# Performance work log

Measured on AMD Instinct MI355X. Metric: run time of the kernel, lower is better.

## Reference

```python
import jax, jax.numpy as jnp
import numpy as np

NUM_USERS = 60000
NUM_ITEMS = 40000
N_NODES = NUM_USERS + NUM_ITEMS
EMBED_K = 128
E_HALF = 1_000_000  # bipartite interactions; symmetrized -> 2M directed edges


def setup_inputs() -> dict:
    key = jax.random.key(0)
    k1, k2, k3, k4, k5, k6, k7 = jax.random.split(key, 7)
    scale = 1.0 / np.sqrt(EMBED_K)  # ~ xavier_normal
    Gu = jax.random.normal(k1, (NUM_USERS, EMBED_K), jnp.float32) * scale
    Gi = jax.random.normal(k2, (NUM_ITEMS, EMBED_K), jnp.float32) * scale
    W0 = jax.random.normal(k3, (EMBED_K, EMBED_K), jnp.float32) * scale
    W1 = jax.random.normal(k4, (EMBED_K, EMBED_K), jnp.float32) * scale
    W2 = jax.random.normal(k5, (EMBED_K, EMBED_K), jnp.float32) * scale
    # bipartite user-item graph, symmetrized (items offset by NUM_USERS)
    u = jax.random.randint(k6, (E_HALF,), 0, NUM_USERS)
    it = jax.random.randint(k7, (E_HALF,), 0, NUM_ITEMS) + NUM_USERS
    src = jnp.concatenate([u, it])
    dst = jnp.concatenate([it, u])
    edge_index = jnp.stack([src, dst]).astype(jnp.int32)  # [2, 2M]
    return {"Gu": Gu, "Gi": Gi, "W0": W0, "W1": W1, "W2": W2,
            "edge_index": edge_index}


def reference(Gu, Gi, W0, W1, W2, edge_index):
    # add_self_loops=False, bias=False) -> ReLU), then split into (gu, gi).
    src, dst = edge_index[0], edge_index[1]
    n_users = Gu.shape[0]
    n_nodes = Gu.shape[0] + Gi.shape[0]
    # PyG gcn_norm (no self loops): deg = scatter(1, col); norm = d^-1/2[row]*d^-1/2[col]
    ones = jnp.ones(src.shape, Gu.dtype)
    deg = jax.ops.segment_sum(ones, dst, num_segments=n_nodes)
    dinv = jnp.where(deg > 0, jax.lax.rsqrt(jnp.maximum(deg, 1.0)), 0.0)
    norm = dinv[src] * dinv[dst]  # [E]
    x = jnp.concatenate([Gu, Gi], axis=0)  # [N, d]
    for W in (W0, W1, W2):
        h = x @ W                                   # [N, d] dense GEMM
        msg = h[src] * norm[:, None]                # [E, d] gather + scale
        x = jax.nn.relu(jax.ops.segment_sum(msg, dst, num_segments=n_nodes))
    return x[:n_users], x[n_users:]
```

## Files before the change

kernel.cpp:

```cpp
#include <hip/hip_runtime.h>
#include <hip/hip_bf16.h>

#define EMB 128
#define NPB 256
#define NB_PAD 512
#define CHUNK 4096
#define FILL_CAP 7168

typedef unsigned int uint32;
typedef unsigned long long uint64;
typedef __attribute__((ext_vector_type(8))) short bf16x8;
typedef __attribute__((ext_vector_type(4))) float f32x4;
typedef __attribute__((ext_vector_type(2))) float f32x2;
typedef __attribute__((ext_vector_type(2))) unsigned int uint32x2;

__device__ __forceinline__ ushort f2bf(float f) {
    uint32 u = __float_as_uint(f);
    return (ushort)((u + 0x7fff + ((u >> 16) & 1)) >> 16);
}
__device__ __forceinline__ uint32 pack_hi2(uint32 u0, uint32 u1) {
    return (u1 & 0xffff0000u) | (u0 >> 16);
}
__device__ __forceinline__ float blo(uint32 u) { return __uint_as_float(u << 16); }
__device__ __forceinline__ float bhi(uint32 u) { return __uint_as_float(u & 0xffff0000u); }


__global__ __launch_bounds__(256) void bucket_count_kernel(
    const int* __restrict__ dst, int* __restrict__ bucket_cnt, int E, int NB) {
    __shared__ int cnt[NB_PAD];
    int t = threadIdx.x;
    long e0 = (long)blockIdx.x * CHUNK;
    int n = E - (int)e0; if (n > CHUNK) n = CHUNK;
    for (int b = t; b < NB_PAD; b += 256) cnt[b] = 0;
    __syncthreads();
    #pragma unroll
    for (int i = 0; i < CHUNK / 256; i++) {
        int idx = t + i * 256;
        if (idx < n) atomicAdd(&cnt[dst[e0 + idx] >> 8], 1);
    }
    __syncthreads();
    for (int b = t; b < NB; b += 256)
        if (cnt[b] > 0) atomicAdd(&bucket_cnt[b], cnt[b]);
}

__global__ void bucket_scan_kernel(const int* __restrict__ bucket_cnt,
                                   int* __restrict__ ebase, int* __restrict__ gcursor,
                                   int NB, int E) {
    __shared__ int sc[512];
    int t = threadIdx.x;
    int v = (t < NB) ? bucket_cnt[t] : 0;
    sc[t] = v;
    __syncthreads();
    for (int off = 1; off < 512; off <<= 1) {
        int u = (t >= off) ? sc[t - off] : 0;
        __syncthreads();
        sc[t] += u;
        __syncthreads();
    }
    if (t < NB) {
        int excl = sc[t] - v;
        ebase[t] = excl;
        gcursor[t] = excl;
    }
    if (t == 0) ebase[NB] = E;
}


__global__ __launch_bounds__(256) void bucket_scatter_kernel(
    const int* __restrict__ src, const int* __restrict__ dst,
    int* __restrict__ gcursor, uint2* __restrict__ ebuf, int E, int NB) {
    __shared__ int cnt[NB_PAD];
    __shared__ int loff[NB_PAD];
    __shared__ int gbase[NB_PAD];
    __shared__ int pos[NB_PAD];
    __shared__ int sc[256];
    __shared__ uint2 stage[CHUNK];
    int t = threadIdx.x;
    long e0 = (long)blockIdx.x * CHUNK;
    int n = E - (int)e0; if (n > CHUNK) n = CHUNK;
    for (int b = t; b < NB_PAD; b += 256) { cnt[b] = 0; pos[b] = 0; }
    __syncthreads();
    int es[CHUNK / 256], ed[CHUNK / 256];
    #pragma unroll
    for (int i = 0; i < CHUNK / 256; i++) {
        int idx = t + i * 256;
        if (idx < n) {
            es[i] = src[e0 + idx];
            ed[i] = dst[e0 + idx];
            atomicAdd(&cnt[ed[i] >> 8], 1);
        }
    }
    __syncthreads();
    int a = cnt[2 * t], b2 = cnt[2 * t + 1];
    sc[t] = a + b2;
    __syncthreads();
    for (int off = 1; off < 256; off <<= 1) {
        int v = (t >= off) ? sc[t - off] : 0;
        __syncthreads();
        sc[t] += v;
        __syncthreads();
    }
    int excl = sc[t] - (a + b2);
    loff[2 * t] = excl;
    loff[2 * t + 1] = excl + a;
    __syncthreads();
    for (int b = t; b < NB; b += 256)
        if (cnt[b] > 0) gbase[b] = atomicAdd(&gcursor[b], cnt[b]);
    __syncthreads();
    #pragma unroll
    for (int i = 0; i < CHUNK / 256; i++) {
        int idx = t + i * 256;
        if (idx < n) {
            int b = ed[i] >> 8;
            int p = atomicAdd(&pos[b], 1);
            stage[loff[b] + p] = make_uint2((uint32)es[i], (uint32)ed[i]);
        }
    }
    __syncthreads();
    for (int i = t; i < n; i += 256) {
        uint2 e = stage[i];
        int b = (int)e.y >> 8;
        ebuf[gbase[b] + (i - loff[b])] = e;
    }
}


__global__ __launch_bounds__(256) void bucket_deg_kernel(
    const uint2* __restrict__ ebuf, const int* __restrict__ ebase,
    int* __restrict__ deg, float* __restrict__ dinv, int N) {
    __shared__ int cnt[NPB];
    int t = threadIdx.x;
    int n0 = blockIdx.x * NPB;
    int nn = N - n0; if (nn > NPB) nn = NPB;
    cnt[t] = 0;
    __syncthreads();
    int e0 = ebase[blockIdx.x];
    int e1 = ebase[blockIdx.x + 1];
    for (int e = e0 + t; e < e1; e += 256) {
        uint2 sd = ebuf[e];
        atomicAdd(&cnt[(int)sd.y - n0], 1);
    }
    __syncthreads();
    if (t < nn) {
        int c = cnt[t];
        deg[n0 + t] = c;
        dinv[n0 + t] = c > 0 ? rsqrtf((float)c) : 0.0f;
    }
}


__global__ void scan1_kernel(const int* __restrict__ deg, int* __restrict__ rowptr,
                             int* __restrict__ bsum, int N) {
    __shared__ int sc[256];
    int t = threadIdx.x;
    int base = blockIdx.x * 1024 + t * 4;
    int d0 = 0, d1 = 0, d2 = 0, d3 = 0;
    if (base + 3 < N) {
        int4 v = *(const int4*)(deg + base);
        d0 = v.x; d1 = v.y; d2 = v.z; d3 = v.w;
    } else {
        if (base     < N) d0 = deg[base];
        if (base + 1 < N) d1 = deg[base + 1];
        if (base + 2 < N) d2 = deg[base + 2];
        if (base + 3 < N) d3 = deg[base + 3];
    }
    int s = d0 + d1 + d2 + d3;
    sc[t] = s;
    __syncthreads();
    for (int off = 1; off < 256; off <<= 1) {
        int v = (t >= off) ? sc[t - off] : 0;
        __syncthreads();
        sc[t] += v;
        __syncthreads();
    }
    int excl = sc[t] - s;
    if (t == 255) bsum[blockIdx.x] = sc[255];
    int dd[4] = {d0, d1, d2, d3};
    int p = excl;
    #pragma unroll
    for (int j = 0; j < 4; j++) {
        int i = base + j;
        if (i < N) rowptr[i] = p;
        p += dd[j];
    }
}

__global__ void scan2_kernel(int* bsum, int nb) {
    __shared__ int sc[128];
    int t = threadIdx.x;
    int v = (t < nb) ? bsum[t] : 0;
    sc[t] = v;
    __syncthreads();
    for (int off = 1; off < 128; off <<= 1) {
        int u = (t >= off) ? sc[t - off] : 0;
        __syncthreads();
        sc[t] += u;
        __syncthreads();
    }
    if (t < nb) bsum[t] = sc[t] - v;
}

__global__ void scan3_kernel(int* __restrict__ rowptr, const int* __restrict__ bsum,
                             int N, int E) {
    int t = threadIdx.x, b = blockIdx.x;
    int add = bsum[b];
    int base = b * 1024 + t * 4;
    #pragma unroll
    for (int j = 0; j < 4; j++) {
        int i = base + j;
        if (i < N) rowptr[i] += add;
    }
    if (b == 0 && t == 0) rowptr[N] = E;
}


__global__ __launch_bounds__(256) void fill_ew_kernel(
    uint2* __restrict__ ebuf, const int* __restrict__ rowptr,
    const float* __restrict__ dinv, int N) {
    __shared__ uint2 stage[FILL_CAP];
    __shared__ int cnt[NPB];
    __shared__ int rp[NPB];
    int t = threadIdx.x;
    int n0 = blockIdx.x * NPB;
    int nn = N - n0; if (nn > NPB) nn = NPB;
    if (t < nn) { cnt[t] = 0; rp[t] = rowptr[n0 + t]; }
    __syncthreads();
    int e0 = rowptr[n0];
    int e1 = rowptr[n0 + nn];
    int ecount = e1 - e0; if (ecount > FILL_CAP) ecount = FILL_CAP;
    for (int o = t; o < ecount; o += 256) stage[o] = ebuf[e0 + o];
    __syncthreads();
    for (int o = t; o < ecount; o += 1024) {
        uint2 sd[4]; int pos[4]; float wv[4];
        int valid = 0;
        #pragma unroll
        for (int k = 0; k < 4; k++) {
            int oo = o + k * 256;
            if (oo < ecount) { sd[k] = stage[oo]; valid = k + 1; }
        }
        #pragma unroll
        for (int k = 0; k < 4; k++)
            if (k < valid) {
                int local = (int)sd[k].y - n0;
                pos[k] = rp[local] + atomicAdd(&cnt[local], 1);
            }
        #pragma unroll
        for (int k = 0; k < 4; k++)
            if (k < valid) wv[k] = dinv[(int)sd[k].x];
        #pragma unroll
        for (int k = 0; k < 4; k++)
            if (k < valid) ebuf[pos[k]] = make_uint2(sd[k].x, __float_as_uint(wv[k]));
    }
}


template<int DI>
__device__ __forceinline__ void agg_tail2(
    const uint32x2* __restrict__ Yh2, const uint2* __restrict__ ew,
    int base, int e0, int e1, int half, int l32,
    float& a0, float& a1, float& a2, float& a3) {
    uint32 rows[DI]; float w[DI]; uint32x2 p[DI];
    #pragma unroll
    for (int k = 0; k < DI; k++) {
        int i0 = base + 2 * k, i1 = i0 + 1;
        uint2 s0 = ew[i0 < e1 ? i0 : e0];
        uint2 s1 = ew[i1 < e1 ? i1 : e0];
        rows[k] = half ? s1.x : s0.x;
        uint32 wu = half ? s1.y : s0.y;
        w[k] = (i0 + half < e1) ? __uint_as_float(wu) : 0.0f;
    }
    #pragma unroll
    for (int k = 0; k < DI; k++) p[k] = Yh2[(size_t)rows[k] * 32 + l32];
    #pragma unroll
    for (int k = 0; k < DI; k++) {
        a0 += w[k] * blo(p[k].x); a1 += w[k] * bhi(p[k].x);
        a2 += w[k] * blo(p[k].y); a3 += w[k] * bhi(p[k].y);
    }
}

__device__ __forceinline__ void agg_node2(
    const uint32x2* __restrict__ Yh2, const uint2* __restrict__ ew,
    int e0, int e1, int half, int l32,
    float& a0, float& a1, float& a2, float& a3) {
    int base = e0;
    for (; base + 16 <= e1; base += 16) {
        uint32 rows[8]; float w[8]; uint32x2 p[8];
        #pragma unroll
        for (int k = 0; k < 8; k++) {
            uint2 s0 = ew[base + 2 * k];
            uint2 s1 = ew[base + 2 * k + 1];
            rows[k] = half ? s1.x : s0.x;
            w[k] = __uint_as_float(half ? s1.y : s0.y);
        }
        #pragma unroll
        for (int k = 0; k < 8; k++) p[k] = Yh2[(size_t)rows[k] * 32 + l32];
        #pragma unroll
        for (int k = 0; k < 8; k++) {
            a0 += w[k] * blo(p[k].x); a1 += w[k] * bhi(p[k].x);
            a2 += w[k] * blo(p[k].y); a3 += w[k] * bhi(p[k].y);
        }
    }
    int rem = e1 - base;
    if (rem > 8)      agg_tail2<8>(Yh2, ew, base, e0, e1, half, l32, a0, a1, a2, a3);
    else if (rem > 4) agg_tail2<4>(Yh2, ew, base, e0, e1, half, l32, a0, a1, a2, a3);
    else if (rem > 2) agg_tail2<2>(Yh2, ew, base, e0, e1, half, l32, a0, a1, a2, a3);
    else if (rem > 0) agg_tail2<1>(Yh2, ew, base, e0, e1, half, l32, a0, a1, a2, a3);
}

__global__ __launch_bounds__(256) void agg_relu_kernel(
    const uint32x2* __restrict__ Yh2,
    const int* __restrict__ rowptr, const uint2* __restrict__ ew,
    const float* __restrict__ dinv, float* __restrict__ out, int N) {
    int node = blockIdx.x * 4 + (threadIdx.x >> 6);
    if (node >= N) return;
    int lane = threadIdx.x & 63;
    int half = lane >> 5, l32 = lane & 31;
    int e0 = __builtin_amdgcn_readfirstlane(rowptr[node]);
    int e1 = __builtin_amdgcn_readfirstlane(rowptr[node + 1]);
    float a0 = 0.f, a1 = 0.f, a2 = 0.f, a3 = 0.f;
    agg_node2(Yh2, ew, e0, e1, half, l32, a0, a1, a2, a3);
    a0 += __shfl_xor(a0, 32);
    a1 += __shfl_xor(a1, 32);
    a2 += __shfl_xor(a2, 32);
    a3 += __shfl_xor(a3, 32);
    if (half == 0) {
        float wd = dinv[node];
        f32x4 r = { fmaxf(a0 * wd, 0.f), fmaxf(a1 * wd, 0.f),
                    fmaxf(a2 * wd, 0.f), fmaxf(a3 * wd, 0.f) };
        __builtin_nontemporal_store(r, (f32x4*)(out + (size_t)node * EMB + l32 * 4));
    }
}


__global__ void wsplit_kernel(const float* __restrict__ W0, const float* __restrict__ W1,
                              const float* __restrict__ W2,
                              ushort* __restrict__ Whi, ushort* __restrict__ Wlo) {
    const float* W = (blockIdx.x == 0) ? W0 : (blockIdx.x == 1) ? W1 : W2;
    ushort* hiT = Whi + blockIdx.x * EMB * EMB;
    ushort* loT = Wlo + blockIdx.x * EMB * EMB;
    for (int i = threadIdx.x; i < EMB * EMB; i += blockDim.x) {
        int k = i >> 7, n = i & 127;
        float w = W[i];
        uint32 u = __float_as_uint(w);
        ushort hi = (ushort)(u >> 16);
        float hif = __uint_as_float(u & 0xffff0000u);
        ushort lo = f2bf(w - hif);
        hiT[n * EMB + k] = hi;
        loT[n * EMB + k] = lo;
    }
}


union FragU { uint32 u[4]; bf16x8 v; };

__global__ __launch_bounds__(256, 2) void gemm_mfma_kernel(
    const float* __restrict__ A, const float* __restrict__ A2, int Msplit,
    const ushort* __restrict__ WhiT, const ushort* __restrict__ WloT,
    ushort* __restrict__ Yh, int M) {
    __shared__ float As[16][132];
    int t = threadIdx.x;
    int wv = t >> 6, lane = t & 63, quad = lane >> 4, l16 = lane & 15;

    FragU bfr[8][2];
    #pragma unroll
    for (int kc = 0; kc < 8; kc++) {
        const ushort* srcW = (kc < 4) ? WhiT : WloT;
        int kb = (kc & 3) * 32 + quad * 8;
        #pragma unroll
        for (int c = 0; c < 2; c++) {
            int n = wv * 32 + c * 16 + l16;
            const uint32* p = (const uint32*)(srcW + n * EMB + kb);
            bfr[kc][c].u[0] = p[0];
            bfr[kc][c].u[1] = p[1];
            bfr[kc][c].u[2] = p[2];
            bfr[kc][c].u[3] = p[3];
        }
    }

    int srow = t >> 4, skq = t & 15;
    int ntile = (M + 15) >> 4;
    for (int tile = blockIdx.x; tile < ntile; tile += (int)gridDim.x) {
        int r0 = tile << 4;
        __syncthreads();
        {
            float4 v0 = {0.f, 0.f, 0.f, 0.f}, v1 = v0;
            int row = r0 + srow;
            if (row < M) {
                const float* ga = (row < Msplit)
                    ? A  + (size_t)row * EMB + skq * 8
                    : A2 + (size_t)(row - Msplit) * EMB + skq * 8;
                v0 = *(const float4*)ga;
                v1 = *(const float4*)(ga + 4);
            }
            *(float4*)&As[srow][skq * 8] = v0;
            *(float4*)&As[srow][skq * 8 + 4] = v1;
        }
        __syncthreads();

        FragU ah[4], al[4];
        #pragma unroll
        for (int kc = 0; kc < 4; kc++) {
            const float* p = &As[l16][kc * 32 + quad * 8];
            float4 xa = *(const float4*)p;
            float4 xb = *(const float4*)(p + 4);
            uint32 u0 = __float_as_uint(xa.x), u1 = __float_as_uint(xa.y);
            uint32 u2 = __float_as_uint(xa.z), u3 = __float_as_uint(xa.w);
            uint32 u4 = __float_as_uint(xb.x), u5 = __float_as_uint(xb.y);
            uint32 u6 = __float_as_uint(xb.z), u7 = __float_as_uint(xb.w);
            ah[kc].u[0] = pack_hi2(u0, u1);
            ah[kc].u[1] = pack_hi2(u2, u3);
            ah[kc].u[2] = pack_hi2(u4, u5);
            ah[kc].u[3] = pack_hi2(u6, u7);
            float l0 = xa.x - __uint_as_float(u0 & 0xffff0000u);
            float l1 = xa.y - __uint_as_float(u1 & 0xffff0000u);
            float l2 = xa.z - __uint_as_float(u2 & 0xffff0000u);
            float l3 = xa.w - __uint_as_float(u3 & 0xffff0000u);
            float l4 = xb.x - __uint_as_float(u4 & 0xffff0000u);
            float l5 = xb.y - __uint_as_float(u5 & 0xffff0000u);
            float l6 = xb.z - __uint_as_float(u6 & 0xffff0000u);
            float l7 = xb.w - __uint_as_float(u7 & 0xffff0000u);
            al[kc].u[0] = pack_hi2(__float_as_uint(l0), __float_as_uint(l1));
            al[kc].u[1] = pack_hi2(__float_as_uint(l2), __float_as_uint(l3));
            al[kc].u[2] = pack_hi2(__float_as_uint(l4), __float_as_uint(l5));
            al[kc].u[3] = pack_hi2(__float_as_uint(l6), __float_as_uint(l7));
        }

        f32x4 acc0 = {0.f, 0.f, 0.f, 0.f};
        f32x4 acc1 = {0.f, 0.f, 0.f, 0.f};
        #pragma unroll
        for (int kc = 0; kc < 4; kc++) {
            acc0 = __builtin_amdgcn_mfma_f32_16x16x32_bf16(ah[kc].v, bfr[kc][0].v, acc0, 0, 0, 0);
            acc1 = __builtin_amdgcn_mfma_f32_16x16x32_bf16(ah[kc].v, bfr[kc][1].v, acc1, 0, 0, 0);
        }
        #pragma unroll
        for (int kc = 0; kc < 4; kc++) {
            acc0 = __builtin_amdgcn_mfma_f32_16x16x32_bf16(ah[kc].v, bfr[kc + 4][0].v, acc0, 0, 0, 0);
            acc1 = __builtin_amdgcn_mfma_f32_16x16x32_bf16(ah[kc].v, bfr[kc + 4][1].v, acc1, 0, 0, 0);
        }
        #pragma unroll
        for (int kc = 0; kc < 4; kc++) {
            acc0 = __builtin_amdgcn_mfma_f32_16x16x32_bf16(al[kc].v, bfr[kc][0].v, acc0, 0, 0, 0);
            acc1 = __builtin_amdgcn_mfma_f32_16x16x32_bf16(al[kc].v, bfr[kc][1].v, acc1, 0, 0, 0);
        }

        int colb = wv * 32 + l16;
        #pragma unroll
        for (int r = 0; r < 4; r++) {
            int row = r0 + quad * 4 + r;
            if (row < M) {
                Yh[(size_t)row * EMB + colb]      = f2bf(acc0[r]);
                Yh[(size_t)row * EMB + colb + 16] = f2bf(acc1[r]);
            }
        }
    }
}


extern "C" void kernel_launch(void* const* d_in, const int* in_sizes, int n_in,
                              void* d_out, int out_size, void* d_ws, size_t ws_size,
                              hipStream_t stream) {
    (void)n_in; (void)out_size; (void)ws_size;
    const float* Gu = (const float*)d_in[0];
    const float* Gi = (const float*)d_in[1];
    const float* W0 = (const float*)d_in[2];
    const float* W1 = (const float*)d_in[3];
    const float* W2 = (const float*)d_in[4];
    const int* ei = (const int*)d_in[5];

    int nu = in_sizes[0] / EMB;
    int ni = in_sizes[1] / EMB;
    int N = nu + ni;
    int E = in_sizes[5] / 2;
    const int* src = ei;
    const int* dst = ei + E;
    int NB = (N + NPB - 1) / NPB;

    ushort* Yh      = (ushort*)d_ws;
    uint2* ebuf     = (uint2*)(Yh + (size_t)N * EMB);
    int* deg        = (int*)(ebuf + (size_t)E);
    int* rowptr     = deg + N;
    float* dinv     = (float*)(rowptr + N + 1);
    int* bucket_cnt = (int*)(dinv + N);
    int* ebase      = bucket_cnt + NB;
    int* gcursor    = ebase + NB + 1;
    int* bsum       = gcursor + NB;
    ushort* WhiT    = (ushort*)(bsum + 128);
    ushort* WloT    = WhiT + 3 * EMB * EMB;
    float* X        = (float*)d_out;

    (void)hipMemsetAsync(bucket_cnt, 0, sizeof(int) * (size_t)NB, stream);

    wsplit_kernel<<<3, 256, 0, stream>>>(W0, W1, W2, WhiT, WloT);

    int ecb = (E + CHUNK - 1) / CHUNK;
    bucket_count_kernel<<<ecb, 256, 0, stream>>>(dst, bucket_cnt, E, NB);
    bucket_scan_kernel<<<1, 512, 0, stream>>>(bucket_cnt, ebase, gcursor, NB, E);
    bucket_scatter_kernel<<<ecb, 256, 0, stream>>>(src, dst, gcursor, ebuf, E, NB);
    bucket_deg_kernel<<<NB, 256, 0, stream>>>(ebuf, ebase, deg, dinv, N);
    int nb = (N + 1023) / 1024;
    scan1_kernel<<<nb, 256, 0, stream>>>(deg, rowptr, bsum, N);
    scan2_kernel<<<1, 128, 0, stream>>>(bsum, nb);
    scan3_kernel<<<nb, 256, 0, stream>>>(rowptr, bsum, N, E);
    fill_ew_kernel<<<NB, 256, 0, stream>>>(ebuf, rowptr, dinv, N);

    const uint2* ew = (const uint2*)ebuf;
    int aggBlocks = (N + 3) / 4;
    const int GB = 512;

    gemm_mfma_kernel<<<GB, 256, 0, stream>>>(Gu, Gi, nu, WhiT, WloT, Yh, N);
    agg_relu_kernel<<<aggBlocks, 256, 0, stream>>>((const uint32x2*)Yh, rowptr, ew, dinv, X, N);
    gemm_mfma_kernel<<<GB, 256, 0, stream>>>(X, X, N, WhiT + EMB * EMB, WloT + EMB * EMB, Yh, N);
    agg_relu_kernel<<<aggBlocks, 256, 0, stream>>>((const uint32x2*)Yh, rowptr, ew, dinv, X, N);
    gemm_mfma_kernel<<<GB, 256, 0, stream>>>(X, X, N, WhiT + 2 * EMB * EMB, WloT + 2 * EMB * EMB, Yh, N);
    agg_relu_kernel<<<aggBlocks, 256, 0, stream>>>((const uint32x2*)Yh, rowptr, ew, dinv, X, N);
}
```

Measured before the change: 466.8 us.

## Fuse degree count with per-bucket scan and fold memset into wsplit

Each destination bucket already knows its global edge offset, so rowptr is now computed inside bucket_deg_kernel with a local block scan. This removes the three-kernel global scan and the separate deg array. The bucket_cnt memset is folded into the weight-split kernel, and that kernel now runs on 48 blocks instead of 3 to spread its work. The goal is fewer launches and less serialized small work, at the cost of an extra shared-memory scan in the degree kernel.

```diff
diff --git a/kernel.cpp b/kernel.cpp
--- a/kernel.cpp
+++ b/kernel.cpp
@@ -23,6 +23,34 @@
 }
 __device__ __forceinline__ float blo(uint32 u) { return __uint_as_float(u << 16); }
 __device__ __forceinline__ float bhi(uint32 u) { return __uint_as_float(u & 0xffff0000u); }
+
+
+__global__ __launch_bounds__(256) void wsplit_kernel(
+    const float* __restrict__ W0, const float* __restrict__ W1,
+    const float* __restrict__ W2,
+    ushort* __restrict__ Whi, ushort* __restrict__ Wlo,
+    int* __restrict__ bucket_cnt, int NB) {
+    int wsel = blockIdx.x >> 4, part = blockIdx.x & 15;
+    if (blockIdx.x == 0) {
+        for (int b = threadIdx.x; b < NB; b += 256) bucket_cnt[b] = 0;
+    }
+    const float* W = (wsel == 0) ? W0 : (wsel == 1) ? W1 : W2;
+    ushort* hiT = Whi + wsel * EMB * EMB;
+    ushort* loT = Wlo + wsel * EMB * EMB;
+    int i0 = part * 1024;
+    #pragma unroll
+    for (int j = 0; j < 4; j++) {
+        int i = i0 + threadIdx.x + j * 256;
+        int k = i >> 7, n = i & 127;
+        float w = W[i];
+        uint32 u = __float_as_uint(w);
+        ushort hi = (ushort)(u >> 16);
+        float hif = __uint_as_float(u & 0xffff0000u);
+        ushort lo = f2bf(w - hif);
+        hiT[n * EMB + k] = hi;
+        loT[n * EMB + k] = lo;
+    }
+}
 
 
 __global__ __launch_bounds__(256) void bucket_count_kernel(
@@ -127,8 +155,9 @@
 
 __global__ __launch_bounds__(256) void bucket_deg_kernel(
     const uint2* __restrict__ ebuf, const int* __restrict__ ebase,
-    int* __restrict__ deg, float* __restrict__ dinv, int N) {
+    int* __restrict__ rowptr, float* __restrict__ dinv, int N, int E) {
     __shared__ int cnt[NPB];
+    __shared__ int sc[256];
     int t = threadIdx.x;
     int n0 = blockIdx.x * NPB;
     int nn = N - n0; if (nn > NPB) nn = NPB;
@@ -141,31 +170,8 @@
         atomicAdd(&cnt[(int)sd.y - n0], 1);
     }
     __syncthreads();
-    if (t < nn) {
-        int c = cnt[t];
-        deg[n0 + t] = c;
-        dinv[n0 + t] = c > 0 ? rsqrtf((float)c) : 0.0f;
-    }
-}
-
-
-__global__ void scan1_kernel(const int* __restrict__ deg, int* __restrict__ rowptr,
-                             int* __restrict__ bsum, int N) {
-    __shared__ int sc[256];
-    int t = threadIdx.x;
-    int base = blockIdx.x * 1024 + t * 4;
-    int d0 = 0, d1 = 0, d2 = 0, d3 = 0;
-    if (base + 3 < N) {
-        int4 v = *(const int4*)(deg + base);
-        d0 = v.x; d1 = v.y; d2 = v.z; d3 = v.w;
-    } else {
-        if (base     < N) d0 = deg[base];
-        if (base + 1 < N) d1 = deg[base + 1];
-        if (base + 2 < N) d2 = deg[base + 2];
-        if (base + 3 < N) d3 = deg[base + 3];
-    }
-    int s = d0 + d1 + d2 + d3;
-    sc[t] = s;
+    int c = cnt[t];
+    sc[t] = c;
     __syncthreads();
     for (int off = 1; off < 256; off <<= 1) {
         int v = (t >= off) ? sc[t - off] : 0;
@@ -173,44 +179,12 @@
         sc[t] += v;
         __syncthreads();
     }
-    int excl = sc[t] - s;
-    if (t == 255) bsum[blockIdx.x] = sc[255];
-    int dd[4] = {d0, d1, d2, d3};
-    int p = excl;
-    #pragma unroll
-    for (int j = 0; j < 4; j++) {
-        int i = base + j;
-        if (i < N) rowptr[i] = p;
-        p += dd[j];
-    }
-}
-
-__global__ void scan2_kernel(int* bsum, int nb) {
-    __shared__ int sc[128];
-    int t = threadIdx.x;
-    int v = (t < nb) ? bsum[t] : 0;
-    sc[t] = v;
-    __syncthreads();
-    for (int off = 1; off < 128; off <<= 1) {
-        int u = (t >= off) ? sc[t - off] : 0;
-        __syncthreads();
-        sc[t] += u;
-        __syncthreads();
-    }
-    if (t < nb) bsum[t] = sc[t] - v;
-}
-
-__global__ void scan3_kernel(int* __restrict__ rowptr, const int* __restrict__ bsum,
-                             int N, int E) {
-    int t = threadIdx.x, b = blockIdx.x;
-    int add = bsum[b];
-    int base = b * 1024 + t * 4;
-    #pragma unroll
-    for (int j = 0; j < 4; j++) {
-        int i = base + j;
-        if (i < N) rowptr[i] += add;
-    }
-    if (b == 0 && t == 0) rowptr[N] = E;
+    int excl = sc[t] - c;
+    if (t < nn) {
+        rowptr[n0 + t] = e0 + excl;
+        dinv[n0 + t] = c > 0 ? rsqrtf((float)c) : 0.0f;
+    }
+    if (t == 0 && n0 + nn == N) rowptr[N] = E;
 }
 
 
@@ -328,25 +302,6 @@
         f32x4 r = { fmaxf(a0 * wd, 0.f), fmaxf(a1 * wd, 0.f),
                     fmaxf(a2 * wd, 0.f), fmaxf(a3 * wd, 0.f) };
         __builtin_nontemporal_store(r, (f32x4*)(out + (size_t)node * EMB + l32 * 4));
-    }
-}
-
-
-__global__ void wsplit_kernel(const float* __restrict__ W0, const float* __restrict__ W1,
-                              const float* __restrict__ W2,
-                              ushort* __restrict__ Whi, ushort* __restrict__ Wlo) {
-    const float* W = (blockIdx.x == 0) ? W0 : (blockIdx.x == 1) ? W1 : W2;
-    ushort* hiT = Whi + blockIdx.x * EMB * EMB;
-    ushort* loT = Wlo + blockIdx.x * EMB * EMB;
-    for (int i = threadIdx.x; i < EMB * EMB; i += blockDim.x) {
-        int k = i >> 7, n = i & 127;
-        float w = W[i];
-        uint32 u = __float_as_uint(w);
-        ushort hi = (ushort)(u >> 16);
-        float hif = __uint_as_float(u & 0xffff0000u);
-        ushort lo = f2bf(w - hif);
-        hiT[n * EMB + k] = hi;
-        loT[n * EMB + k] = lo;
     }
 }
 
@@ -477,30 +432,22 @@
 
     ushort* Yh      = (ushort*)d_ws;
     uint2* ebuf     = (uint2*)(Yh + (size_t)N * EMB);
-    int* deg        = (int*)(ebuf + (size_t)E);
-    int* rowptr     = deg + N;
+    int* rowptr     = (int*)(ebuf + (size_t)E);
     float* dinv     = (float*)(rowptr + N + 1);
     int* bucket_cnt = (int*)(dinv + N);
     int* ebase      = bucket_cnt + NB;
     int* gcursor    = ebase + NB + 1;
-    int* bsum       = gcursor + NB;
-    ushort* WhiT    = (ushort*)(bsum + 128);
+    ushort* WhiT    = (ushort*)(gcursor + NB);
     ushort* WloT    = WhiT + 3 * EMB * EMB;
     float* X        = (float*)d_out;
 
-    (void)hipMemsetAsync(bucket_cnt, 0, sizeof(int) * (size_t)NB, stream);
-
-    wsplit_kernel<<<3, 256, 0, stream>>>(W0, W1, W2, WhiT, WloT);
+    wsplit_kernel<<<48, 256, 0, stream>>>(W0, W1, W2, WhiT, WloT, bucket_cnt, NB);
 
     int ecb = (E + CHUNK - 1) / CHUNK;
     bucket_count_kernel<<<ecb, 256, 0, stream>>>(dst, bucket_cnt, E, NB);
     bucket_scan_kernel<<<1, 512, 0, stream>>>(bucket_cnt, ebase, gcursor, NB, E);
     bucket_scatter_kernel<<<ecb, 256, 0, stream>>>(src, dst, gcursor, ebuf, E, NB);
-    bucket_deg_kernel<<<NB, 256, 0, stream>>>(ebuf, ebase, deg, dinv, N);
-    int nb = (N + 1023) / 1024;
-    scan1_kernel<<<nb, 256, 0, stream>>>(deg, rowptr, bsum, N);
-    scan2_kernel<<<1, 128, 0, stream>>>(bsum, nb);
-    scan3_kernel<<<nb, 256, 0, stream>>>(rowptr, bsum, N, E);
+    bucket_deg_kernel<<<NB, 256, 0, stream>>>(ebuf, ebase, rowptr, dinv, N, E);
     fill_ew_kernel<<<NB, 256, 0, stream>>>(ebuf, rowptr, dinv, N);
 
     const uint2* ew = (const uint2*)ebuf;
```

Result: faster. 428.2 us (-8.3%).
